# Kernel tuning notes

Measured on AMD Instinct MI355X. Metric: run time of the kernel, lower is better.

## Reference

```python
import jax, jax.numpy as jnp
import numpy as np

B, S, D, H = 2, 2048, 1024, 16
HD = D // H
SPARSITY = 0.1
LAMBDA_MAX = 10.0
ALPHA = 5.0


def local_prior_mask(seq_len: int, sparsity: float) -> jnp.ndarray:
    # |i - j| <= window_size // 2, window_size = int(seq_len * sparsity)
    window_size = max(1, int(seq_len * sparsity))
    rows = jnp.arange(seq_len)[:, None]
    cols = jnp.arange(seq_len)[None, :]
    return jnp.abs(rows - cols) <= (window_size // 2)


def setup_inputs() -> dict:
    key = jax.random.key(0)
    ks = jax.random.split(key, 12)
    scale = 1.0 / np.sqrt(D)
    inp = {
        'x': jax.random.normal(ks[0], (B, S, D), dtype=jnp.float32),
        'u_prev': jax.random.uniform(ks[1], (B, 1), dtype=jnp.float32),
        'Wq': jax.random.normal(ks[2], (D, D), dtype=jnp.float32) * scale,
        'bq': jnp.zeros((D,), dtype=jnp.float32),
        'Wk': jax.random.normal(ks[3], (D, D), dtype=jnp.float32) * scale,
        'bk': jnp.zeros((D,), dtype=jnp.float32),
        'Wv': jax.random.normal(ks[4], (D, D), dtype=jnp.float32) * scale,
        'bv': jnp.zeros((D,), dtype=jnp.float32),
        'Wo': jax.random.normal(ks[5], (D, D), dtype=jnp.float32) * scale,
        'bo': jnp.zeros((D,), dtype=jnp.float32),
    }
    return inp


def reference(x, u_prev, Wq, bq, Wk, bk, Wv, bv, Wo, bo):
    b, s, _ = x.shape
    # projections (torch Linear: y = x W^T + b)
    def proj(W, bias):
        return (x @ W.T + bias).reshape(b, s, H, HD).transpose(0, 2, 1, 3)  # [B,H,S,HD]
    q = proj(Wq, bq)
    k = proj(Wk, bk)
    v = proj(Wv, bv)

    # dynamic gating: lambda = lambda_max * exp(-alpha * u_prev), shape [B,1,1,1]
    lam = (LAMBDA_MAX * jnp.exp(-ALPHA * u_prev)).reshape(b, 1, 1, 1)

    prior = local_prior_mask(s, SPARSITY)  # [S,S] bool

    scores = jnp.einsum('bhqd,bhkd->bhqk', q, k) / jnp.sqrt(jnp.asarray(HD, x.dtype))
    # additive prior bias: penalize positions outside the structural prior by -lambda
    scores = scores - lam * (~prior).astype(x.dtype)

    attn = jax.nn.softmax(scores, axis=-1)
    out = jnp.einsum('bhqk,bhkd->bhqd', attn, v)           # [B,H,S,HD]
    out = out.transpose(0, 2, 1, 3).reshape(b, s, D)        # [B,S,D]
    out = out @ Wo.T + bo
    return out, lam.reshape(b, 1)
```

## Files before the change

kernel.cpp:

```cpp
#include <hip/hip_runtime.h>

typedef __attribute__((ext_vector_type(8))) short short8;
typedef __attribute__((ext_vector_type(4))) float f32x4;

#define MFMA16(a,b,c) __builtin_amdgcn_mfma_f32_16x16x32_bf16(a,b,c,0,0,0)

__device__ __forceinline__ unsigned short f2bf(float f){
  unsigned int u = __float_as_uint(f);
  u += 0x7FFF + ((u>>16)&1);
  return (unsigned short)(u>>16);
}

__device__ __forceinline__ float fexp2(float x){
#if __has_builtin(__builtin_amdgcn_exp2f)
  return __builtin_amdgcn_exp2f(x);
#else
  return exp2f(x);
#endif
}

__device__ __forceinline__ void gl_lds16(const void* g, void* l){
  __builtin_amdgcn_global_load_lds((const __attribute__((address_space(1))) void*)g,
                                   (__attribute__((address_space(3))) void*)l, 16, 0, 0);
}

__global__ void cvt_bf16(const float* __restrict__ src, unsigned short* __restrict__ dst, int n){
  int i = (blockIdx.x*blockDim.x + threadIdx.x)*4;
  if (i + 3 < n){
    float4 v = *(const float4*)(src + i);
    ushort4 o;
    o.x = f2bf(v.x); o.y = f2bf(v.y); o.z = f2bf(v.z); o.w = f2bf(v.w);
    *(ushort4*)(dst + i) = o;
  }
}

template<int MODE>
__global__ __launch_bounds__(256) void gemm_bt(
  const unsigned short* __restrict__ A,
  const unsigned short* __restrict__ Bw,
  const float* __restrict__ bias0, const float* __restrict__ bias1, const float* __restrict__ bias2,
  unsigned short* __restrict__ Qo, unsigned short* __restrict__ Ko, unsigned short* __restrict__ VTo,
  float* __restrict__ Co,
  int M, int N, int K)
{
  __shared__ unsigned short As[2][128*32];
  __shared__ unsigned short Bs[2][128*32];
  const int tid = threadIdx.x;
  const int m0 = blockIdx.y*128, n0 = blockIdx.x*128;
  const int w = tid>>6, lane = tid&63, lr = lane&15, lg = lane>>4;
  const int wm = w>>1, wn = w&1;
  const int nk = K/32;

  auto stage = [&](int buf, int kt){
    const unsigned short* Ag = A + (size_t)m0*K + kt*32;
    const unsigned short* Bg = Bw + (size_t)n0*K + kt*32;
    #pragma unroll
    for (int it=0; it<2; ++it){
      int slot = it*256 + tid;
      gl_lds16(Ag + (size_t)(slot>>2)*K + (slot&3)*8, &As[buf][slot*8]);
    }
    #pragma unroll
    for (int it=0; it<2; ++it){
      int slot = it*256 + tid;
      gl_lds16(Bg + (size_t)(slot>>2)*K + (slot&3)*8, &Bs[buf][slot*8]);
    }
  };

  f32x4 acc[4][4] = {};
  stage(0,0);
  for (int kt=0; kt<nk; ++kt){
    int cur = kt&1;
    __syncthreads();
    if (kt+1 < nk) stage(cur^1, kt+1);
    short8 af[4], bfr[4];
    #pragma unroll
    for (int i=0;i<4;++i) af[i]  = *(const short8*)&As[cur][(wm*64 + i*16 + lr)*32 + lg*8];
    #pragma unroll
    for (int j=0;j<4;++j) bfr[j] = *(const short8*)&Bs[cur][(wn*64 + j*16 + lr)*32 + lg*8];
    #pragma unroll
    for (int i=0;i<4;++i)
      #pragma unroll
      for (int j=0;j<4;++j)
        acc[i][j] = MFMA16(af[i], bfr[j], acc[i][j]);
  }

  #pragma unroll
  for (int i=0;i<4;++i){
    #pragma unroll
    for (int j=0;j<4;++j){
      const int n  = n0 + wn*64 + j*16 + lr;
      const int mb = m0 + wm*64 + i*16 + lg*4;
      if (MODE==0){
        const int which = n>>10, nn = n&1023;
        const float bv = (which==0) ? bias0[nn] : (which==1) ? bias1[nn] : bias2[nn];
        const int h = nn>>6, hd = nn&63;
        #pragma unroll
        for (int r=0;r<4;++r){
          const int m = mb + r;
          const int b = m>>11, s = m&2047;
          const unsigned short u = f2bf(acc[i][j][r] + bv);
          const size_t bh = (size_t)(b*16 + h);
          if (which==0)      Qo[(bh*2048 + s)*64 + hd] = u;
          else if (which==1) Ko[(bh*2048 + s)*64 + hd] = u;
          else               VTo[(bh*64 + hd)*2048 + s] = u;
        }
      } else {
        const float bv = bias0[n];
        #pragma unroll
        for (int r=0;r<4;++r){
          const int m = mb + r;
          Co[(size_t)m*N + n] = acc[i][j][r] + bv;
        }
      }
    }
  }
}

__global__ __launch_bounds__(256, 4) void attn_k(
  const unsigned short* __restrict__ Qb,
  const unsigned short* __restrict__ Kb,
  const unsigned short* __restrict__ VT,
  const float* __restrict__ u_prev,
  unsigned short* __restrict__ Out)
{
  const int qt = blockIdx.x, bh = blockIdx.y;
  const int b = bh>>4, h = bh&15;
  const float lam = 10.f * __expf(-5.f * u_prev[b]);
  const float nlamb = -lam * 1.4426950408889634f;
  const int tid = threadIdx.x;
  const int w = tid>>6, lane = tid&63, lr = lane&15, lg = lane>>4;
  const int q0 = qt*64 + w*16;

  const unsigned short* Qp = Qb + (size_t)bh*2048*64;
  const unsigned short* Kp = Kb + (size_t)bh*2048*64;
  const unsigned short* Vp = VT + (size_t)bh*64*2048;

  __shared__ unsigned short Ks[2][2048];
  __shared__ unsigned short Vs[2][2048];
  __shared__ unsigned short p_lds[4][16][40];

  auto stage = [&](int buf, int kt){
    const int k0 = kt*32;
    gl_lds16(Kp + (size_t)(k0 + (tid&31))*64 + (tid>>5)*8, &Ks[buf][tid*8]);
    gl_lds16(Vp + (size_t)(tid&63)*2048 + k0 + (tid>>6)*8, &Vs[buf][tid*8]);
  };

  short8 qf0 = *(const short8*)&Qp[(size_t)(q0+lr)*64 +      lg*8];
  short8 qf1 = *(const short8*)&Qp[(size_t)(q0+lr)*64 + 32 + lg*8];

  const float c1 = 0.18033688011112042f;

  float l_run[4] = {0.f, 0.f, 0.f, 0.f};
  f32x4 o0 = {}, o1 = {}, o2 = {}, o3 = {};

  stage(0, 0);
  for (int kt=0; kt<64; ++kt){
    const int cur = kt&1;
    __syncthreads();
    if (kt+1 < 64) stage(cur^1, kt+1);

    const unsigned short* Kc = Ks[cur];
    const unsigned short* Vc = Vs[cur];
    short8 k00 = *(const short8*)&Kc[(lg*32 +      lr)*8];
    short8 k01 = *(const short8*)&Kc[1024 + (lg*32 +      lr)*8];
    short8 k10 = *(const short8*)&Kc[(lg*32 + 16 + lr)*8];
    short8 k11 = *(const short8*)&Kc[1024 + (lg*32 + 16 + lr)*8];
    short8 vf0 = *(const short8*)&Vc[(lg*64 +      lr)*8];
    short8 vf1 = *(const short8*)&Vc[(lg*64 + 16 + lr)*8];
    short8 vf2 = *(const short8*)&Vc[(lg*64 + 32 + lr)*8];
    short8 vf3 = *(const short8*)&Vc[(lg*64 + 48 + lr)*8];

    f32x4 s0 = {}, s1 = {};
    s0 = MFMA16(qf0, k00, s0); s0 = MFMA16(qf1, k01, s0);
    s1 = MFMA16(qf0, k10, s1); s1 = MFMA16(qf1, k11, s1);

    const int k0_ = kt*32;
    const int cls_ = (k0_ > q0 + 117 || k0_ < q0 - 133) ? 2
                   : (k0_ >= q0 - 87 && k0_ <= q0 + 71) ? 0 : 1;
    #pragma unroll
    for (int r=0;r<4;++r){
      const int qi_ = q0 + lg*4 + r;
      float b0 = 0.f, b1 = 0.f;
      if (cls_ == 2){ b0 = nlamb; b1 = nlamb; }
      else if (cls_ == 1){
        int d0 = qi_ - (k0_ + lr);      if (d0<0) d0 = -d0;
        int d1 = qi_ - (k0_ + 16 + lr); if (d1<0) d1 = -d1;
        if (d0 > 102) b0 = nlamb;
        if (d1 > 102) b1 = nlamb;
      }
      const float p0 = fexp2(fmaf(s0[r], c1, b0));
      const float p1 = fexp2(fmaf(s1[r], c1, b1));
      l_run[r] += p0 + p1;
      p_lds[w][lg*4+r][lr]      = f2bf(p0);
      p_lds[w][lg*4+r][16 + lr] = f2bf(p1);
    }
    short8 pa = *(const short8*)&p_lds[w][lr][lg*8];
    o0 = MFMA16(pa, vf0, o0);
    o1 = MFMA16(pa, vf1, o1);
    o2 = MFMA16(pa, vf2, o2);
    o3 = MFMA16(pa, vf3, o3);
  }

  #pragma unroll
  for (int off=1; off<16; off<<=1)
    #pragma unroll
    for (int r=0;r<4;++r)
      l_run[r] += __shfl_xor(l_run[r], off, 64);

  #pragma unroll
  for (int r=0;r<4;++r){
    const int qi = q0 + lg*4 + r;
    const float linv = 1.0f / l_run[r];
    unsigned short* op = &Out[((size_t)b*2048 + qi)*1024 + h*64 + lr];
    op[0]  = f2bf(o0[r] * linv);
    op[16] = f2bf(o1[r] * linv);
    op[32] = f2bf(o2[r] * linv);
    op[48] = f2bf(o3[r] * linv);
  }
}

__global__ void tail_k(const float* __restrict__ u, float* __restrict__ out){
  int i = threadIdx.x;
  if (i < 2) out[4194304 + i] = 10.f*__expf(-5.f*u[i]);
}

extern "C" void kernel_launch(void* const* d_in, const int* in_sizes, int n_in,
                              void* d_out, int out_size, void* d_ws, size_t ws_size,
                              hipStream_t stream){
  const float* x  = (const float*)d_in[0];
  const float* u  = (const float*)d_in[1];
  const float* Wq = (const float*)d_in[2];
  const float* bq = (const float*)d_in[3];
  const float* Wk = (const float*)d_in[4];
  const float* bk = (const float*)d_in[5];
  const float* Wv = (const float*)d_in[6];
  const float* bv = (const float*)d_in[7];
  const float* Wo = (const float*)d_in[8];
  const float* bo = (const float*)d_in[9];
  float* out = (float*)d_out;

  unsigned char* ws = (unsigned char*)d_ws;
  unsigned short* xb    = (unsigned short*)(ws);
  unsigned short* attnb = xb;
  unsigned short* Wqkvb = (unsigned short*)(ws + 8388608);
  unsigned short* Wob   = (unsigned short*)(ws + 14680064);
  unsigned short* Qb2   = (unsigned short*)(ws + 16777216);
  unsigned short* Kb2   = (unsigned short*)(ws + 25165824);
  unsigned short* VTb   = (unsigned short*)(ws + 33554432);

  cvt_bf16<<<4096, 256, 0, stream>>>(x,  xb, 4194304);
  cvt_bf16<<<1024, 256, 0, stream>>>(Wq, Wqkvb,            1048576);
  cvt_bf16<<<1024, 256, 0, stream>>>(Wk, Wqkvb + 1048576,  1048576);
  cvt_bf16<<<1024, 256, 0, stream>>>(Wv, Wqkvb + 2097152,  1048576);
  cvt_bf16<<<1024, 256, 0, stream>>>(Wo, Wob, 1048576);

  gemm_bt<0><<<dim3(24,32), 256, 0, stream>>>(xb, Wqkvb, bq, bk, bv,
                                              Qb2, Kb2, VTb, nullptr, 4096, 3072, 1024);
  attn_k<<<dim3(32,32), 256, 0, stream>>>(Qb2, Kb2, VTb, u, attnb);
  gemm_bt<1><<<dim3(8,32), 256, 0, stream>>>(attnb, Wob, bo, nullptr, nullptr,
                                             nullptr, nullptr, nullptr, out, 4096, 1024, 1024);
  tail_k<<<1, 64, 0, stream>>>(u, out);
}
```

Baseline: 166.6 us.

## Process two query tiles per attention block to reuse staged K/V tiles

```diff
diff --git a/kernel.cpp b/kernel.cpp
--- a/kernel.cpp
+++ b/kernel.cpp
@@ -116,7 +116,7 @@
   }
 }
 
-__global__ __launch_bounds__(256, 4) void attn_k(
+__global__ __launch_bounds__(256, 2) void attn_k(
   const unsigned short* __restrict__ Qb,
   const unsigned short* __restrict__ Kb,
   const unsigned short* __restrict__ VT,
@@ -129,7 +129,8 @@
   const float nlamb = -lam * 1.4426950408889634f;
   const int tid = threadIdx.x;
   const int w = tid>>6, lane = tid&63, lr = lane&15, lg = lane>>4;
-  const int q0 = qt*64 + w*16;
+  const int q0A = qt*128 + w*16;
+  const int q0B = q0A + 64;
 
   const unsigned short* Qp = Qb + (size_t)bh*2048*64;
   const unsigned short* Kp = Kb + (size_t)bh*2048*64;
@@ -137,7 +138,7 @@
 
   __shared__ unsigned short Ks[2][2048];
   __shared__ unsigned short Vs[2][2048];
-  __shared__ unsigned short p_lds[4][16][40];
+  __shared__ unsigned short p_lds[4][2][16][40];
 
   auto stage = [&](int buf, int kt){
     const int k0 = kt*32;
@@ -145,13 +146,16 @@
     gl_lds16(Vp + (size_t)(tid&63)*2048 + k0 + (tid>>6)*8, &Vs[buf][tid*8]);
   };
 
-  short8 qf0 = *(const short8*)&Qp[(size_t)(q0+lr)*64 +      lg*8];
-  short8 qf1 = *(const short8*)&Qp[(size_t)(q0+lr)*64 + 32 + lg*8];
+  short8 qfA0 = *(const short8*)&Qp[(size_t)(q0A+lr)*64 +      lg*8];
+  short8 qfA1 = *(const short8*)&Qp[(size_t)(q0A+lr)*64 + 32 + lg*8];
+  short8 qfB0 = *(const short8*)&Qp[(size_t)(q0B+lr)*64 +      lg*8];
+  short8 qfB1 = *(const short8*)&Qp[(size_t)(q0B+lr)*64 + 32 + lg*8];
 
   const float c1 = 0.18033688011112042f;
 
-  float l_run[4] = {0.f, 0.f, 0.f, 0.f};
-  f32x4 o0 = {}, o1 = {}, o2 = {}, o3 = {};
+  float lA[4] = {0.f,0.f,0.f,0.f}, lB[4] = {0.f,0.f,0.f,0.f};
+  f32x4 oA0 = {}, oA1 = {}, oA2 = {}, oA3 = {};
+  f32x4 oB0 = {}, oB1 = {}, oB2 = {}, oB3 = {};
 
   stage(0, 0);
   for (int kt=0; kt<64; ++kt){
@@ -170,52 +174,92 @@
     short8 vf2 = *(const short8*)&Vc[(lg*64 + 32 + lr)*8];
     short8 vf3 = *(const short8*)&Vc[(lg*64 + 48 + lr)*8];
 
-    f32x4 s0 = {}, s1 = {};
-    s0 = MFMA16(qf0, k00, s0); s0 = MFMA16(qf1, k01, s0);
-    s1 = MFMA16(qf0, k10, s1); s1 = MFMA16(qf1, k11, s1);
-
     const int k0_ = kt*32;
-    const int cls_ = (k0_ > q0 + 117 || k0_ < q0 - 133) ? 2
-                   : (k0_ >= q0 - 87 && k0_ <= q0 + 71) ? 0 : 1;
-    #pragma unroll
-    for (int r=0;r<4;++r){
-      const int qi_ = q0 + lg*4 + r;
-      float b0 = 0.f, b1 = 0.f;
-      if (cls_ == 2){ b0 = nlamb; b1 = nlamb; }
-      else if (cls_ == 1){
-        int d0 = qi_ - (k0_ + lr);      if (d0<0) d0 = -d0;
-        int d1 = qi_ - (k0_ + 16 + lr); if (d1<0) d1 = -d1;
-        if (d0 > 102) b0 = nlamb;
-        if (d1 > 102) b1 = nlamb;
+
+    {
+      f32x4 s0 = {}, s1 = {};
+      s0 = MFMA16(qfA0, k00, s0); s0 = MFMA16(qfA1, k01, s0);
+      s1 = MFMA16(qfA0, k10, s1); s1 = MFMA16(qfA1, k11, s1);
+      const int cls_ = (k0_ > q0A + 117 || k0_ < q0A - 133) ? 2
+                     : (k0_ >= q0A - 87 && k0_ <= q0A + 71) ? 0 : 1;
+      #pragma unroll
+      for (int r=0;r<4;++r){
+        const int qi_ = q0A + lg*4 + r;
+        float b0 = 0.f, b1 = 0.f;
+        if (cls_ == 2){ b0 = nlamb; b1 = nlamb; }
+        else if (cls_ == 1){
+          int d0 = qi_ - (k0_ + lr);      if (d0<0) d0 = -d0;
+          int d1 = qi_ - (k0_ + 16 + lr); if (d1<0) d1 = -d1;
+          if (d0 > 102) b0 = nlamb;
+          if (d1 > 102) b1 = nlamb;
+        }
+        const float p0 = fexp2(fmaf(s0[r], c1, b0));
+        const float p1 = fexp2(fmaf(s1[r], c1, b1));
+        lA[r] += p0 + p1;
+        p_lds[w][0][lg*4+r][lr]      = (unsigned short)(__float_as_uint(p0)>>16);
+        p_lds[w][0][lg*4+r][16 + lr] = (unsigned short)(__float_as_uint(p1)>>16);
       }
-      const float p0 = fexp2(fmaf(s0[r], c1, b0));
-      const float p1 = fexp2(fmaf(s1[r], c1, b1));
-      l_run[r] += p0 + p1;
-      p_lds[w][lg*4+r][lr]      = f2bf(p0);
-      p_lds[w][lg*4+r][16 + lr] = f2bf(p1);
-    }
-    short8 pa = *(const short8*)&p_lds[w][lr][lg*8];
-    o0 = MFMA16(pa, vf0, o0);
-    o1 = MFMA16(pa, vf1, o1);
-    o2 = MFMA16(pa, vf2, o2);
-    o3 = MFMA16(pa, vf3, o3);
+      short8 pa = *(const short8*)&p_lds[w][0][lr][lg*8];
+      oA0 = MFMA16(pa, vf0, oA0);
+      oA1 = MFMA16(pa, vf1, oA1);
+      oA2 = MFMA16(pa, vf2, oA2);
+      oA3 = MFMA16(pa, vf3, oA3);
+    }
+    {
+      f32x4 s0 = {}, s1 = {};
+      s0 = MFMA16(qfB0, k00, s0); s0 = MFMA16(qfB1, k01, s0);
+      s1 = MFMA16(qfB0, k10, s1); s1 = MFMA16(qfB1, k11, s1);
+      const int cls_ = (k0_ > q0B + 117 || k0_ < q0B - 133) ? 2
+                     : (k0_ >= q0B - 87 && k0_ <= q0B + 71) ? 0 : 1;
+      #pragma unroll
+      for (int r=0;r<4;++r){
+        const int qi_ = q0B + lg*4 + r;
+        float b0 = 0.f, b1 = 0.f;
+        if (cls_ == 2){ b0 = nlamb; b1 = nlamb; }
+        else if (cls_ == 1){
+          int d0 = qi_ - (k0_ + lr);      if (d0<0) d0 = -d0;
+          int d1 = qi_ - (k0_ + 16 + lr); if (d1<0) d1 = -d1;
+          if (d0 > 102) b0 = nlamb;
+          if (d1 > 102) b1 = nlamb;
+        }
+        const float p0 = fexp2(fmaf(s0[r], c1, b0));
+        const float p1 = fexp2(fmaf(s1[r], c1, b1));
+        lB[r] += p0 + p1;
+        p_lds[w][1][lg*4+r][lr]      = (unsigned short)(__float_as_uint(p0)>>16);
+        p_lds[w][1][lg*4+r][16 + lr] = (unsigned short)(__float_as_uint(p1)>>16);
+      }
+      short8 pa = *(const short8*)&p_lds[w][1][lr][lg*8];
+      oB0 = MFMA16(pa, vf0, oB0);
+      oB1 = MFMA16(pa, vf1, oB1);
+      oB2 = MFMA16(pa, vf2, oB2);
+      oB3 = MFMA16(pa, vf3, oB3);
+    }
   }
 
   #pragma unroll
   for (int off=1; off<16; off<<=1)
     #pragma unroll
-    for (int r=0;r<4;++r)
-      l_run[r] += __shfl_xor(l_run[r], off, 64);
+    for (int r=0;r<4;++r){
+      lA[r] += __shfl_xor(lA[r], off, 64);
+      lB[r] += __shfl_xor(lB[r], off, 64);
+    }
 
   #pragma unroll
   for (int r=0;r<4;++r){
-    const int qi = q0 + lg*4 + r;
-    const float linv = 1.0f / l_run[r];
-    unsigned short* op = &Out[((size_t)b*2048 + qi)*1024 + h*64 + lr];
-    op[0]  = f2bf(o0[r] * linv);
-    op[16] = f2bf(o1[r] * linv);
-    op[32] = f2bf(o2[r] * linv);
-    op[48] = f2bf(o3[r] * linv);
+    const int qiA = q0A + lg*4 + r;
+    const float liA = 1.0f / lA[r];
+    unsigned short* opA = &Out[((size_t)b*2048 + qiA)*1024 + h*64 + lr];
+    opA[0]  = f2bf(oA0[r] * liA);
+    opA[16] = f2bf(oA1[r] * liA);
+    opA[32] = f2bf(oA2[r] * liA);
+    opA[48] = f2bf(oA3[r] * liA);
+    const int qiB = q0B + lg*4 + r;
+    const float liB = 1.0f / lB[r];
+    unsigned short* opB = &Out[((size_t)b*2048 + qiB)*1024 + h*64 + lr];
+    opB[0]  = f2bf(oB0[r] * liB);
+    opB[16] = f2bf(oB1[r] * liB);
+    opB[32] = f2bf(oB2[r] * liB);
+    opB[48] = f2bf(oB3[r] * liB);
   }
 }
 
@@ -256,7 +300,7 @@
 
   gemm_bt<0><<<dim3(24,32), 256, 0, stream>>>(xb, Wqkvb, bq, bk, bv,
                                               Qb2, Kb2, VTb, nullptr, 4096, 3072, 1024);
-  attn_k<<<dim3(32,32), 256, 0, stream>>>(Qb2, Kb2, VTb, u, attnb);
+  attn_k<<<dim3(16,32), 256, 0, stream>>>(Qb2, Kb2, VTb, u, attnb);
   gemm_bt<1><<<dim3(8,32), 256, 0, stream>>>(attnb, Wob, bo, nullptr, nullptr,
                                              nullptr, nullptr, nullptr, out, 4096, 1024, 1024);
   tail_k<<<1, 64, 0, stream>>>(u, out);
```

New measurement: 171.1 us. 2.7% more time.
